# Kernel optimization log

Hardware: AMD Instinct MI355X
Metric: run time of the kernel (lower is better)

The kernel has to match this reference:

```python
import jax, jax.numpy as jnp
import numpy as np

C = 512
NUM_HEADS = 4
GROUPS = 32
EPS = 1e-5


def setup_inputs() -> dict:
    key = jax.random.key(0)
    ks = jax.random.split(key, 7)
    x = jax.random.normal(ks[0], (1, C, 4, 32, 32), dtype=jnp.float32)
    norm_w = jax.random.normal(ks[1], (C,), dtype=jnp.float32) * 0.02 + 1.0
    norm_b = jax.random.normal(ks[2], (C,), dtype=jnp.float32) * 0.02
    # 1x1x1 Conv3d == pointwise linear over channels
    qkv_w = jax.random.normal(ks[3], (3 * C, C), dtype=jnp.float32) * (C ** -0.5)
    qkv_b = jax.random.normal(ks[4], (3 * C,), dtype=jnp.float32) * 0.02
    proj_w = jax.random.normal(ks[5], (C, C), dtype=jnp.float32) * (C ** -0.5)
    proj_b = jax.random.normal(ks[6], (C,), dtype=jnp.float32) * 0.02
    return {"x": x, "norm_w": norm_w, "norm_b": norm_b,
            "qkv_w": qkv_w, "qkv_b": qkv_b,
            "proj_w": proj_w, "proj_b": proj_b}


def reference(x, norm_w, norm_b, qkv_w, qkv_b, proj_w, proj_b):
    B, Cc, T, H, W = x.shape
    N = T * H * W
    nh = NUM_HEADS
    d = Cc // nh
    # GroupNorm(32, C), biased variance, eps=1e-5
    xg = x.reshape(B, GROUPS, Cc // GROUPS, N)
    mu = xg.mean(axis=(2, 3), keepdims=True)
    var = xg.var(axis=(2, 3), keepdims=True)
    h = ((xg - mu) * jax.lax.rsqrt(var + EPS)).reshape(B, Cc, N)
    h = h * norm_w[None, :, None] + norm_b[None, :, None]
    # QKV 1x1 conv as channel matmul: (B, 3C, N)
    qkv = jnp.einsum('oc,bcn->bon', qkv_w, h) + qkv_b[None, :, None]
    qkv = qkv.reshape(B, 3, nh, d, N)
    q, k, v = qkv[:, 0], qkv[:, 1], qkv[:, 2]  # each (B, nh, d, N)
    scale = d ** -0.5
    attn = jax.nn.softmax(jnp.einsum('bhdn,bhdm->bhnm', q, k) * scale, axis=-1)
    out = jnp.einsum('bhnm,bhdm->bhdn', attn, v).reshape(B, Cc, N)
    out = jnp.einsum('oc,bcn->bon', proj_w, out) + proj_b[None, :, None]
    return x + out.reshape(B, Cc, T, H, W)
```

## Files before the change

kernel.cpp:

```cpp
#include <hip/hip_runtime.h>
#include <hip/hip_bf16.h>

#define CDIM 512
#define NTOK 4096
#define NH 4
#define DH 128
#define NGRP 32
#define EPS 1e-5f
#define NSPLIT 4
#define KVBLK 64
#define TPS (NTOK/KVBLK/NSPLIT)

typedef __attribute__((ext_vector_type(8))) short bf16x8;
typedef __attribute__((ext_vector_type(4))) short short4v;
typedef __attribute__((ext_vector_type(4))) float f32x4;
typedef __attribute__((ext_vector_type(16))) float f32x16;

__device__ inline unsigned short f2bf(float f){
  unsigned int u = __float_as_uint(f);
  u = (u + 0x7fffu + ((u >> 16) & 1u)) >> 16;
  return (unsigned short)u;
}

__device__ inline unsigned short f2bf_fast(float f){
  return (unsigned short)((__float_as_uint(f) + 0x8000u) >> 16);
}

__device__ inline float bf2f(unsigned short u){
  return __uint_as_float(((unsigned int)u) << 16);
}

__device__ inline f32x4 mfma_bf16(bf16x8 a, bf16x8 b, f32x4 c){
  asm("v_mfma_f32_16x16x32_bf16 %0, %1, %2, %0" : "+v"(c) : "v"(a), "v"(b));
  return c;
}

__device__ inline f32x16 mfma32(bf16x8 a, bf16x8 b, f32x16 c){
  asm("v_mfma_f32_32x32x16_bf16 %0, %1, %2, %0" : "+v"(c) : "v"(a), "v"(b));
  return c;
}

#define GLD16(gsrc, ldst) \
  __builtin_amdgcn_global_load_lds((__attribute__((address_space(1))) const void*)(gsrc), \
                                   (__attribute__((address_space(3))) void*)(ldst), 16, 0, 0)

#define KSC (0.088388347648318447f * 1.4426950408889634f)
#define INV_KSC (1.0f / KSC)
#define THR_RAW 60.0f
#define THR_K (THR_RAW * KSC)

__global__ __launch_bounds__(256) void k_convert(const float* __restrict__ qkv_w,
                                                 const float* __restrict__ proj_w,
                                                 unsigned short* __restrict__ qw,
                                                 unsigned short* __restrict__ pw){
  int stride = gridDim.x * blockDim.x;
  int i0 = blockIdx.x * blockDim.x + threadIdx.x;
  for (int i = i0; i < 3*CDIM*CDIM; i += stride) qw[i] = f2bf(qkv_w[i]);
  for (int i = i0; i < CDIM*CDIM; i += stride)   pw[i] = f2bf(proj_w[i]);
}

__global__ __launch_bounds__(256) void k_gnstats(const float* __restrict__ x,
                                                 float* __restrict__ stats){
  const int g = blockIdx.x, t = threadIdx.x;
  const f32x4* p = (const f32x4*)(x + (size_t)g * (16*NTOK));
  float s = 0.f, ss = 0.f;
  for (int i = t; i < 16*NTOK/4; i += 256){
    f32x4 v = p[i];
    s  += v[0]+v[1]+v[2]+v[3];
    ss += v[0]*v[0]+v[1]*v[1]+v[2]*v[2]+v[3]*v[3];
  }
  for (int off = 32; off > 0; off >>= 1){ s += __shfl_down(s, off); ss += __shfl_down(ss, off); }
  __shared__ float rs[4], rss[4];
  if ((t & 63) == 0){ rs[t>>6] = s; rss[t>>6] = ss; }
  __syncthreads();
  if (t == 0){
    float S  = rs[0]+rs[1]+rs[2]+rs[3];
    float SS = rss[0]+rss[1]+rss[2]+rss[3];
    const float inv = 1.f / (float)(16*NTOK);
    float mu  = S * inv;
    float var = SS * inv - mu*mu;
    stats[g]        = mu;
    stats[NGRP + g] = rsqrtf(var + EPS);
  }
}

__global__ __launch_bounds__(256) void k_gnapply(const float* __restrict__ x,
                                                 const float* __restrict__ stats,
                                                 const float* __restrict__ nw,
                                                 const float* __restrict__ nbias,
                                                 unsigned short* __restrict__ h_t){
  __shared__ float tile[64][68];
  const int n0 = blockIdx.x * 64, c0 = blockIdx.y * 64;
  const int t = threadIdx.x;
  {
    const int cl = t >> 2;
    #pragma unroll
    for (int i = 0; i < 4; i++){
      const int f4 = (t & 3) + i*4;
      *(f32x4*)&tile[cl][f4*4] = *(const f32x4*)(x + (size_t)(c0+cl)*NTOK + n0 + f4*4);
    }
  }
  __syncthreads();
  const int nl = t >> 2, cb = (t & 3) * 16;
  unsigned short ov[16] __attribute__((aligned(8)));
  #pragma unroll
  for (int j = 0; j < 16; j++){
    const int c = c0 + cb + j;
    const int grp = c >> 4;
    const float val = (tile[cb+j][nl] - stats[grp]) * stats[NGRP+grp] * nw[c] + nbias[c];
    ov[j] = f2bf(val);
  }
  unsigned short* dst = h_t + (size_t)(n0+nl)*CDIM + c0 + cb;
  #pragma unroll
  for (int j = 0; j < 4; j++) *(short4v*)(dst + j*4) = *(const short4v*)(ov + j*4);
}

template<int MODE>
__global__ __launch_bounds__(256) void k_gemm(const unsigned short* __restrict__ A,
                                              const unsigned short* __restrict__ Bt,
                                              const float* __restrict__ bias,
                                              const float* __restrict__ xres,
                                              unsigned short* __restrict__ q_t,
                                              unsigned short* __restrict__ k_t,
                                              unsigned short* __restrict__ vbuf,
                                              float* __restrict__ out,
                                              int K)
{
  __shared__ unsigned short Asm[128*32];
  __shared__ unsigned short Bsm[128*32];
  const int m0 = blockIdx.y * 128, n0 = blockIdx.x * 128;
  const int t = threadIdx.x;
  const int lane = t & 63, w = t >> 6;
  const int lo = lane & 15, g = lane >> 4;
  const int wr = w >> 1, wc = w & 1;
  f32x4 acc[4][4];
  #pragma unroll
  for (int i=0;i<4;i++)
    #pragma unroll
    for (int j=0;j<4;j++) acc[i][j] = f32x4{0.f,0.f,0.f,0.f};

  const int row = t >> 2, cb8 = (t & 3) * 8;
  for (int k0 = 0; k0 < K; k0 += 32){
    __syncthreads();
    *(bf16x8*)(Asm + row*32 + cb8)      = *(const bf16x8*)(A  + (size_t)(m0+row)*K    + k0 + cb8);
    *(bf16x8*)(Asm + (row+64)*32 + cb8) = *(const bf16x8*)(A  + (size_t)(m0+row+64)*K + k0 + cb8);
    *(bf16x8*)(Bsm + row*32 + cb8)      = *(const bf16x8*)(Bt + (size_t)(n0+row)*K    + k0 + cb8);
    *(bf16x8*)(Bsm + (row+64)*32 + cb8) = *(const bf16x8*)(Bt + (size_t)(n0+row+64)*K + k0 + cb8);
    __syncthreads();
    bf16x8 af[4], bfr[4];
    #pragma unroll
    for (int i=0;i<4;i++) af[i]  = *(const bf16x8*)(Asm + (wr*64 + i*16 + lo)*32 + g*8);
    #pragma unroll
    for (int j=0;j<4;j++) bfr[j] = *(const bf16x8*)(Bsm + (wc*64 + j*16 + lo)*32 + g*8);
    #pragma unroll
    for (int i=0;i<4;i++)
      #pragma unroll
      for (int j=0;j<4;j++)
        acc[i][j] = mfma_bf16(af[i], bfr[j], acc[i][j]);
  }

  if constexpr (MODE == 0){
    const int sQ = m0 >> 9;
    const int hh = (m0 >> 7) & 3;
    #pragma unroll
    for (int i=0;i<4;i++){
      const int ddb = wr*64 + i*16 + g*4;
      const int ob  = m0 + ddb;
      float b[4];
      #pragma unroll
      for (int r=0;r<4;r++) b[r] = bias[ob + r];
      #pragma unroll
      for (int j=0;j<4;j++){
        const int n = n0 + wc*64 + j*16 + lo;
        if (sQ < 2){
          unsigned short pk[4] __attribute__((aligned(8)));
          #pragma unroll
          for (int r=0;r<4;r++) pk[r] = f2bf(acc[i][j][r] + b[r]);
          unsigned short* dst = (sQ == 0 ? q_t : k_t) + ((size_t)hh*NTOK + n)*DH + ddb;
          *(short4v*)dst = *(const short4v*)pk;
        } else {
          #pragma unroll
          for (int r=0;r<4;r++)
            vbuf[((size_t)hh*DH + ddb + r)*NTOK + n] = f2bf(acc[i][j][r] + b[r]);
        }
      }
    }
  } else {
    #pragma unroll
    for (int i=0;i<4;i++){
      const int ob = m0 + wr*64 + i*16 + g*4;
      float b[4];
      #pragma unroll
      for (int r=0;r<4;r++) b[r] = bias[ob + r];
      #pragma unroll
      for (int j=0;j<4;j++){
        const int n = n0 + wc*64 + j*16 + lo;
        #pragma unroll
        for (int r=0;r<4;r++){
          size_t idx = (size_t)(ob + r)*NTOK + n;
          out[idx] = acc[i][j][r] + b[r] + xres[idx];
        }
      }
    }
  }
}

__global__ __launch_bounds__(512, 2) void k_attn(const unsigned short* __restrict__ q_t,
                                                 const unsigned short* __restrict__ k_t,
                                                 const unsigned short* __restrict__ vbuf,
                                                 unsigned short* __restrict__ opart,
                                                 float* __restrict__ mlbuf){
  const int h = blockIdx.y;
  const int qt = blockIdx.x >> 2, split = blockIdx.x & 3;
  const int t = threadIdx.x, w = t >> 6, lane = t & 63;
  const int la = lane & 31, hi = lane >> 5;
  const int s15 = la & 15, s7 = la & 7;
  const int nbq = qt * 256 + w * 32;

  __shared__ __align__(16) unsigned short Ksm[2][64*128];
  __shared__ __align__(16) unsigned short Vsm[2][128*64];
  __shared__ __align__(16) unsigned short P[8][32][72];

  const unsigned short* kg = k_t  + (size_t)h*NTOK*DH;
  const unsigned short* vg = vbuf + (size_t)h*DH*NTOK;

  auto stage = [&](int mt, int buf){
    const unsigned short* kgm = kg + (size_t)mt*KVBLK*DH;
    const unsigned short* vgm = vg + mt*KVBLK;
    #pragma unroll
    for (int rnd = 0; rnd < 2; rnd++){
      const int c = rnd*512 + t;
      const int row = c >> 4, col = c & 15;
      GLD16(kgm + (size_t)row*DH + ((col ^ (row & 15))*8), &Ksm[buf][c*8]);
    }
    #pragma unroll
    for (int rnd = 0; rnd < 2; rnd++){
      const int c = rnd*512 + t;
      const int row = c >> 3, col = c & 7;
      GLD16(vgm + (size_t)row*NTOK + ((col ^ (row & 7))*8), &Vsm[buf][c*8]);
    }
  };

  bf16x8 qa[8];
  {
    const unsigned short* qr = q_t + ((size_t)h*NTOK + nbq + la)*DH + hi*8;
    #pragma unroll
    for (int ks=0;ks<8;ks++) qa[ks] = *(const bf16x8*)(qr + ks*16);
  }
  bf16x8 onesf;
  #pragma unroll
  for (int j=0;j<8;j++) onesf[j] = (short)0x3F80;

  float mk[16];
  f32x16 oacc[4], lacc;
  #pragma unroll
  for (int r=0;r<16;r++){ mk[r] = -1e30f; }
  #pragma unroll
  for (int dt=0;dt<4;dt++)
    #pragma unroll
    for (int r=0;r<16;r++) oacc[dt][r] = 0.f;
  #pragma unroll
  for (int r=0;r<16;r++) lacc[r] = 0.f;

  const int mt0 = split * TPS;
  stage(mt0, 0);
  int cur = 0;
  for (int it = 0; it < TPS; it++){
    __syncthreads();
    if (it + 1 < TPS) stage(mt0 + it + 1, cur ^ 1);

    const unsigned short* Ks = Ksm[cur];
    const unsigned short* Vs = Vsm[cur];

    f32x16 s0, s1;
    #pragma unroll
    for (int r=0;r<16;r++){ s0[r] = 0.f; s1[r] = 0.f; }
    #pragma unroll
    for (int ks=0; ks<8; ks++){
      const int kc = ((2*ks + hi) ^ s15) * 8;
      bf16x8 kf0 = *(const bf16x8*)(Ks + la*128 + kc);
      bf16x8 kf1 = *(const bf16x8*)(Ks + (32+la)*128 + kc);
      s0 = mfma32(qa[ks], kf0, s0);
      s1 = mfma32(qa[ks], kf1, s1);
    }
    float tmax = s0[0];
    #pragma unroll
    for (int r=1;r<16;r++) tmax = fmaxf(tmax, s0[r]);
    #pragma unroll
    for (int r=0;r<16;r++) tmax = fmaxf(tmax, s1[r]);
    #pragma unroll
    for (int off=1; off<64; off<<=1) tmax = fmaxf(tmax, __shfl_xor(tmax, off));
    float mmink = mk[0];
    #pragma unroll
    for (int r=1;r<16;r++) mmink = fminf(mmink, mk[r]);
    if (!__all(tmax * KSC <= mmink + THR_K)){
      float rmax[16];
      #pragma unroll
      for (int r=0;r<16;r++) rmax[r] = fmaxf(s0[r], s1[r]);
      #pragma unroll
      for (int off=1; off<32; off<<=1)
        #pragma unroll
        for (int r=0;r<16;r++) rmax[r] = fmaxf(rmax[r], __shfl_xor(rmax[r], off));
      #pragma unroll
      for (int r=0;r<16;r++){
        float mold = mk[r] * INV_KSC;
        float mn   = fmaxf(mold, rmax[r]);
        float mnk  = mn * KSC;
        float al   = exp2f(mk[r] - mnk);
        mk[r] = mnk;
        lacc[r] *= al;
        #pragma unroll
        for (int dt=0;dt<4;dt++) oacc[dt][r] *= al;
      }
    }
    unsigned short* Pw = &P[w][0][0];
    #pragma unroll
    for (int r=0;r<16;r++){
      const int q = (r&3) + 8*(r>>2) + 4*hi;
      float p0 = exp2f(fmaf(s0[r], KSC, -mk[r]));
      float p1 = exp2f(fmaf(s1[r], KSC, -mk[r]));
      Pw[q*72 + la]      = f2bf_fast(p0);
      Pw[q*72 + 32 + la] = f2bf_fast(p1);
    }
    bf16x8 pa[4];
    #pragma unroll
    for (int kst=0;kst<4;kst++)
      pa[kst] = *(const bf16x8*)(&P[w][la][kst*16 + hi*8]);
    #pragma unroll
    for (int kst=0;kst<4;kst++) lacc = mfma32(pa[kst], onesf, lacc);
    #pragma unroll
    for (int dt=0; dt<4; dt++){
      const int vbase = (dt*32 + la)*64;
      #pragma unroll
      for (int kst=0;kst<4;kst++){
        const int vc = ((2*kst + hi) ^ s7) * 8;
        bf16x8 vf = *(const bf16x8*)(Vs + vbase + vc);
        oacc[dt] = mfma32(pa[kst], vf, oacc[dt]);
      }
    }
    cur ^= 1;
  }
  unsigned short* Od = opart + ((size_t)(split*NH + h)*NTOK + nbq)*DH;
  #pragma unroll
  for (int r=0;r<16;r++){
    const int q = (r&3) + 8*(r>>2) + 4*hi;
    const float linv = 1.f / lacc[r];
    #pragma unroll
    for (int dt=0;dt<4;dt++)
      Od[(size_t)q*DH + dt*32 + la] = f2bf(oacc[dt][r] * linv);
  }
  if (la == 0){
    float* ml = mlbuf + ((size_t)(split*NH + h)*NTOK + nbq)*2;
    #pragma unroll
    for (int r=0;r<16;r++){
      const int q = (r&3) + 8*(r>>2) + 4*hi;
      ml[q*2]     = mk[r] * INV_KSC;
      ml[q*2 + 1] = lacc[r];
    }
  }
}

__global__ __launch_bounds__(256) void k_merge(const unsigned short* __restrict__ opart,
                                               const float* __restrict__ mlbuf,
                                               unsigned short* __restrict__ ao_t){
  const int h = blockIdx.y;
  const int n = blockIdx.x*2 + (threadIdx.x >> 7);
  const int d = threadIdx.x & 127;
  float ms[NSPLIT], ls[NSPLIT], m = -1e30f;
  #pragma unroll
  for (int s=0;s<NSPLIT;s++){
    const float* ml = mlbuf + ((size_t)(s*NH + h)*NTOK + n)*2;
    ms[s] = ml[0]; ls[s] = ml[1];
    m = fmaxf(m, ms[s]);
  }
  float wsum = 0.f, o = 0.f;
  #pragma unroll
  for (int s=0;s<NSPLIT;s++){
    float wgt = exp2f((ms[s]-m)*KSC) * ls[s];
    wsum += wgt;
    o += wgt * bf2f(opart[((size_t)(s*NH + h)*NTOK + n)*DH + d]);
  }
  ao_t[(size_t)n*CDIM + h*DH + d] = f2bf(o / wsum);
}

extern "C" void kernel_launch(void* const* d_in, const int* in_sizes, int n_in,
                              void* d_out, int out_size, void* d_ws, size_t ws_size,
                              hipStream_t stream){
  const float* x      = (const float*)d_in[0];
  const float* norm_w = (const float*)d_in[1];
  const float* norm_b = (const float*)d_in[2];
  const float* qkv_w  = (const float*)d_in[3];
  const float* qkv_b  = (const float*)d_in[4];
  const float* proj_w = (const float*)d_in[5];
  const float* proj_b = (const float*)d_in[6];
  float* out = (float*)d_out;

  char* ws = (char*)d_ws;
  unsigned short* qw  = (unsigned short*)(ws);
  unsigned short* pw  = (unsigned short*)(ws + 1572864);
  unsigned short* h_t = (unsigned short*)(ws + 2097152);
  unsigned short* q_t = (unsigned short*)(ws + 6291456);
  unsigned short* k_t = (unsigned short*)(ws + 10485760);
  unsigned short* vb  = (unsigned short*)(ws + 14680064);
  unsigned short* ao  = (unsigned short*)(ws + 18874368);
  float* stats        = (float*)(ws + 23068672);
  unsigned short* opart = (unsigned short*)(ws + 23072768);
  float* mlbuf        = (float*)(ws + 39849984);

  hipLaunchKernelGGL(k_convert, dim3(1024), dim3(256), 0, stream, qkv_w, proj_w, qw, pw);
  hipLaunchKernelGGL(k_gnstats, dim3(32), dim3(256), 0, stream, x, stats);
  hipLaunchKernelGGL(k_gnapply, dim3(64, 8), dim3(256), 0, stream, x, stats, norm_w, norm_b, h_t);
  hipLaunchKernelGGL((k_gemm<0>), dim3(32, 12), dim3(256), 0, stream,
                     qw, h_t, qkv_b, (const float*)nullptr,
                     q_t, k_t, vb, (float*)nullptr, 512);
  hipLaunchKernelGGL(k_attn, dim3(16*NSPLIT, NH), dim3(512), 0, stream, q_t, k_t, vb, opart, mlbuf);
  hipLaunchKernelGGL(k_merge, dim3(NTOK/2, NH), dim3(256), 0, stream, opart, mlbuf, ao);
  hipLaunchKernelGGL((k_gemm<1>), dim3(32, 4), dim3(256), 0, stream,
                     pw, ao, proj_b, x,
                     (unsigned short*)nullptr, (unsigned short*)nullptr, (unsigned short*)nullptr, out, 512);
}
```

Baseline: 126.6 us.

## Keep attention probabilities in registers via transposed QK and raise KV split count

The attention kernel now computes S^T (K as the A operand) so each lane holds one query column. It packs probabilities to bf16 with v_cvt_pk and a cross-half lane shuffle instead of round-tripping through LDS. This drops the P shared buffer, the ones-vector MFMA row sum and the per-row max shuffles in favour of a per-lane running max and sum. The KV split factor becomes a template parameter that goes to 8 when the workspace allows, and launch bounds allow 4 blocks per CU. The costs are more partial outputs for the merge kernel to combine and register pressure at the higher occupancy target.

```diff
diff --git a/kernel.cpp b/kernel.cpp
--- a/kernel.cpp
+++ b/kernel.cpp
@@ -7,14 +7,13 @@
 #define DH 128
 #define NGRP 32
 #define EPS 1e-5f
-#define NSPLIT 4
 #define KVBLK 64
-#define TPS (NTOK/KVBLK/NSPLIT)
 
 typedef __attribute__((ext_vector_type(8))) short bf16x8;
 typedef __attribute__((ext_vector_type(4))) short short4v;
 typedef __attribute__((ext_vector_type(4))) float f32x4;
 typedef __attribute__((ext_vector_type(16))) float f32x16;
+typedef __attribute__((ext_vector_type(4))) unsigned int u32x4;
 
 __device__ inline unsigned short f2bf(float f){
   unsigned int u = __float_as_uint(f);
@@ -22,10 +21,6 @@
   return (unsigned short)u;
 }
 
-__device__ inline unsigned short f2bf_fast(float f){
-  return (unsigned short)((__float_as_uint(f) + 0x8000u) >> 16);
-}
-
 __device__ inline float bf2f(unsigned short u){
   return __uint_as_float(((unsigned int)u) << 16);
 }
@@ -38,6 +33,12 @@
 __device__ inline f32x16 mfma32(bf16x8 a, bf16x8 b, f32x16 c){
   asm("v_mfma_f32_32x32x16_bf16 %0, %1, %2, %0" : "+v"(c) : "v"(a), "v"(b));
   return c;
+}
+
+__device__ inline unsigned int cvtpk(float lo, float hi){
+  unsigned int r;
+  asm("v_cvt_pk_bf16_f32 %0, %1, %2" : "=v"(r) : "v"(lo), "v"(hi));
+  return r;
 }
 
 #define GLD16(gsrc, ldst) \
@@ -205,13 +206,15 @@
   }
 }
 
-__global__ __launch_bounds__(512, 2) void k_attn(const unsigned short* __restrict__ q_t,
+template<int NS>
+__global__ __launch_bounds__(512, 4) void k_attn(const unsigned short* __restrict__ q_t,
                                                  const unsigned short* __restrict__ k_t,
                                                  const unsigned short* __restrict__ vbuf,
                                                  unsigned short* __restrict__ opart,
                                                  float* __restrict__ mlbuf){
+  const int TPS = NTOK/KVBLK/NS;
   const int h = blockIdx.y;
-  const int qt = blockIdx.x >> 2, split = blockIdx.x & 3;
+  const int qt = blockIdx.x / NS, split = blockIdx.x % NS;
   const int t = threadIdx.x, w = t >> 6, lane = t & 63;
   const int la = lane & 31, hi = lane >> 5;
   const int s15 = la & 15, s7 = la & 7;
@@ -219,7 +222,6 @@
 
   __shared__ __align__(16) unsigned short Ksm[2][64*128];
   __shared__ __align__(16) unsigned short Vsm[2][128*64];
-  __shared__ __align__(16) unsigned short P[8][32][72];
 
   const unsigned short* kg = k_t  + (size_t)h*NTOK*DH;
   const unsigned short* vg = vbuf + (size_t)h*DH*NTOK;
@@ -247,20 +249,14 @@
     #pragma unroll
     for (int ks=0;ks<8;ks++) qa[ks] = *(const bf16x8*)(qr + ks*16);
   }
-  bf16x8 onesf;
-  #pragma unroll
-  for (int j=0;j<8;j++) onesf[j] = (short)0x3F80;
-
-  float mk[16];
-  f32x16 oacc[4], lacc;
-  #pragma unroll
-  for (int r=0;r<16;r++){ mk[r] = -1e30f; }
+
+  float mk = -1e30f;
+  float lsum = 0.f;
+  f32x16 oacc[4];
   #pragma unroll
   for (int dt=0;dt<4;dt++)
     #pragma unroll
     for (int r=0;r<16;r++) oacc[dt][r] = 0.f;
-  #pragma unroll
-  for (int r=0;r<16;r++) lacc[r] = 0.f;
 
   const int mt0 = split * TPS;
   stage(mt0, 0);
@@ -272,110 +268,101 @@
     const unsigned short* Ks = Ksm[cur];
     const unsigned short* Vs = Vsm[cur];
 
-    f32x16 s0, s1;
-    #pragma unroll
-    for (int r=0;r<16;r++){ s0[r] = 0.f; s1[r] = 0.f; }
-    #pragma unroll
-    for (int ks=0; ks<8; ks++){
-      const int kc = ((2*ks + hi) ^ s15) * 8;
-      bf16x8 kf0 = *(const bf16x8*)(Ks + la*128 + kc);
-      bf16x8 kf1 = *(const bf16x8*)(Ks + (32+la)*128 + kc);
-      s0 = mfma32(qa[ks], kf0, s0);
-      s1 = mfma32(qa[ks], kf1, s1);
-    }
-    float tmax = s0[0];
-    #pragma unroll
-    for (int r=1;r<16;r++) tmax = fmaxf(tmax, s0[r]);
-    #pragma unroll
-    for (int r=0;r<16;r++) tmax = fmaxf(tmax, s1[r]);
-    #pragma unroll
-    for (int off=1; off<64; off<<=1) tmax = fmaxf(tmax, __shfl_xor(tmax, off));
-    float mmink = mk[0];
-    #pragma unroll
-    for (int r=1;r<16;r++) mmink = fminf(mmink, mk[r]);
-    if (!__all(tmax * KSC <= mmink + THR_K)){
-      float rmax[16];
-      #pragma unroll
-      for (int r=0;r<16;r++) rmax[r] = fmaxf(s0[r], s1[r]);
-      #pragma unroll
-      for (int off=1; off<32; off<<=1)
+    #pragma unroll
+    for (int half = 0; half < 2; half++){
+      f32x16 s;
+      #pragma unroll
+      for (int r=0;r<16;r++) s[r] = 0.f;
+      #pragma unroll
+      for (int ks=0; ks<8; ks++){
+        bf16x8 kf = *(const bf16x8*)(Ks + (half*32 + la)*128 + (((2*ks + hi) ^ s15) * 8));
+        s = mfma32(kf, qa[ks], s);
+      }
+      float hmax = s[0];
+      #pragma unroll
+      for (int r=1;r<16;r++) hmax = fmaxf(hmax, s[r]);
+      hmax = fmaxf(hmax, __shfl_xor(hmax, 32));
+      const float hk = hmax * KSC;
+      if (!__all(hk <= mk + THR_K)){
+        const float mnk = fmaxf(mk, hk);
+        const float al  = exp2f(mk - mnk);
+        mk = mnk;
+        lsum *= al;
         #pragma unroll
-        for (int r=0;r<16;r++) rmax[r] = fmaxf(rmax[r], __shfl_xor(rmax[r], off));
+        for (int r=0;r<16;r++){
+          const float a = __shfl(al, (r&3) + 8*(r>>2) + 4*hi);
+          #pragma unroll
+          for (int dt=0;dt<4;dt++) oacc[dt][r] *= a;
+        }
+      }
       #pragma unroll
       for (int r=0;r<16;r++){
-        float mold = mk[r] * INV_KSC;
-        float mn   = fmaxf(mold, rmax[r]);
-        float mnk  = mn * KSC;
-        float al   = exp2f(mk[r] - mnk);
-        mk[r] = mnk;
-        lacc[r] *= al;
-        #pragma unroll
-        for (int dt=0;dt<4;dt++) oacc[dt][r] *= al;
-      }
-    }
-    unsigned short* Pw = &P[w][0][0];
-    #pragma unroll
-    for (int r=0;r<16;r++){
-      const int q = (r&3) + 8*(r>>2) + 4*hi;
-      float p0 = exp2f(fmaf(s0[r], KSC, -mk[r]));
-      float p1 = exp2f(fmaf(s1[r], KSC, -mk[r]));
-      Pw[q*72 + la]      = f2bf_fast(p0);
-      Pw[q*72 + 32 + la] = f2bf_fast(p1);
-    }
-    bf16x8 pa[4];
-    #pragma unroll
-    for (int kst=0;kst<4;kst++)
-      pa[kst] = *(const bf16x8*)(&P[w][la][kst*16 + hi*8]);
-    #pragma unroll
-    for (int kst=0;kst<4;kst++) lacc = mfma32(pa[kst], onesf, lacc);
-    #pragma unroll
-    for (int dt=0; dt<4; dt++){
-      const int vbase = (dt*32 + la)*64;
-      #pragma unroll
-      for (int kst=0;kst<4;kst++){
-        const int vc = ((2*kst + hi) ^ s7) * 8;
-        bf16x8 vf = *(const bf16x8*)(Vs + vbase + vc);
-        oacc[dt] = mfma32(pa[kst], vf, oacc[dt]);
+        s[r] = exp2f(fmaf(s[r], KSC, -mk));
+        lsum += s[r];
+      }
+      bf16x8 paf[2];
+      #pragma unroll
+      for (int b=0;b<2;b++){
+        unsigned int A = cvtpk(s[8*b+0], s[8*b+1]);
+        unsigned int B = cvtpk(s[8*b+2], s[8*b+3]);
+        unsigned int C = cvtpk(s[8*b+4], s[8*b+5]);
+        unsigned int D = cvtpk(s[8*b+6], s[8*b+7]);
+        unsigned int E = hi ? A : C;
+        unsigned int F = hi ? B : D;
+        E = (unsigned int)__shfl_xor((int)E, 32);
+        F = (unsigned int)__shfl_xor((int)F, 32);
+        u32x4 m;
+        m[0] = hi ? E : A;
+        m[1] = hi ? F : B;
+        m[2] = hi ? C : E;
+        m[3] = hi ? D : F;
+        paf[b] = __builtin_bit_cast(bf16x8, m);
+      }
+      #pragma unroll
+      for (int dt=0; dt<4; dt++){
+        const int vbase = (dt*32 + la)*64;
+        bf16x8 vf0 = *(const bf16x8*)(Vs + vbase + (((2*(half*2+0) + hi) ^ s7) * 8));
+        bf16x8 vf1 = *(const bf16x8*)(Vs + vbase + (((2*(half*2+1) + hi) ^ s7) * 8));
+        oacc[dt] = mfma32(paf[0], vf0, oacc[dt]);
+        oacc[dt] = mfma32(paf[1], vf1, oacc[dt]);
       }
     }
     cur ^= 1;
   }
+  const float lt = lsum + __shfl_xor(lsum, 32);
   unsigned short* Od = opart + ((size_t)(split*NH + h)*NTOK + nbq)*DH;
   #pragma unroll
   for (int r=0;r<16;r++){
     const int q = (r&3) + 8*(r>>2) + 4*hi;
-    const float linv = 1.f / lacc[r];
+    const float linv = 1.f / __shfl(lt, q);
     #pragma unroll
     for (int dt=0;dt<4;dt++)
       Od[(size_t)q*DH + dt*32 + la] = f2bf(oacc[dt][r] * linv);
   }
-  if (la == 0){
+  if (hi == 0){
     float* ml = mlbuf + ((size_t)(split*NH + h)*NTOK + nbq)*2;
-    #pragma unroll
-    for (int r=0;r<16;r++){
-      const int q = (r&3) + 8*(r>>2) + 4*hi;
-      ml[q*2]     = mk[r] * INV_KSC;
-      ml[q*2 + 1] = lacc[r];
-    }
-  }
-}
-
+    ml[la*2]     = mk * INV_KSC;
+    ml[la*2 + 1] = lt;
+  }
+}
+
+template<int NS>
 __global__ __launch_bounds__(256) void k_merge(const unsigned short* __restrict__ opart,
                                                const float* __restrict__ mlbuf,
                                                unsigned short* __restrict__ ao_t){
   const int h = blockIdx.y;
   const int n = blockIdx.x*2 + (threadIdx.x >> 7);
   const int d = threadIdx.x & 127;
-  float ms[NSPLIT], ls[NSPLIT], m = -1e30f;
-  #pragma unroll
-  for (int s=0;s<NSPLIT;s++){
+  float ms[NS], ls[NS], m = -1e30f;
+  #pragma unroll
+  for (int s=0;s<NS;s++){
     const float* ml = mlbuf + ((size_t)(s*NH + h)*NTOK + n)*2;
     ms[s] = ml[0]; ls[s] = ml[1];
     m = fmaxf(m, ms[s]);
   }
   float wsum = 0.f, o = 0.f;
   #pragma unroll
-  for (int s=0;s<NSPLIT;s++){
+  for (int s=0;s<NS;s++){
     float wgt = exp2f((ms[s]-m)*KSC) * ls[s];
     wsum += wgt;
     o += wgt * bf2f(opart[((size_t)(s*NH + h)*NTOK + n)*DH + d]);
@@ -405,7 +392,6 @@
   unsigned short* ao  = (unsigned short*)(ws + 18874368);
   float* stats        = (float*)(ws + 23068672);
   unsigned short* opart = (unsigned short*)(ws + 23072768);
-  float* mlbuf        = (float*)(ws + 39849984);
 
   hipLaunchKernelGGL(k_convert, dim3(1024), dim3(256), 0, stream, qkv_w, proj_w, qw, pw);
   hipLaunchKernelGGL(k_gnstats, dim3(32), dim3(256), 0, stream, x, stats);
@@ -413,8 +399,21 @@
   hipLaunchKernelGGL((k_gemm<0>), dim3(32, 12), dim3(256), 0, stream,
                      qw, h_t, qkv_b, (const float*)nullptr,
                      q_t, k_t, vb, (float*)nullptr, 512);
-  hipLaunchKernelGGL(k_attn, dim3(16*NSPLIT, NH), dim3(512), 0, stream, q_t, k_t, vb, opart, mlbuf);
-  hipLaunchKernelGGL(k_merge, dim3(NTOK/2, NH), dim3(256), 0, stream, opart, mlbuf, ao);
+
+  if (ws_size >= 57675776ULL){
+    constexpr int NS = 8;
+    float* mlbuf = (float*)(ws + 23072768 + (size_t)NS*NH*NTOK*DH*2);
+    hipLaunchKernelGGL((k_attn<NS>), dim3((NTOK/256)*NS, NH), dim3(512), 0, stream,
+                       q_t, k_t, vb, opart, mlbuf);
+    hipLaunchKernelGGL((k_merge<NS>), dim3(NTOK/2, NH), dim3(256), 0, stream, opart, mlbuf, ao);
+  } else {
+    constexpr int NS = 4;
+    float* mlbuf = (float*)(ws + 23072768 + (size_t)NS*NH*NTOK*DH*2);
+    hipLaunchKernelGGL((k_attn<NS>), dim3((NTOK/256)*NS, NH), dim3(512), 0, stream,
+                       q_t, k_t, vb, opart, mlbuf);
+    hipLaunchKernelGGL((k_merge<NS>), dim3(NTOK/2, NH), dim3(256), 0, stream, opart, mlbuf, ao);
+  }
+
   hipLaunchKernelGGL((k_gemm<1>), dim3(32, 4), dim3(256), 0, stream,
                      pw, ao, proj_b, x,
                      (unsigned short*)nullptr, (unsigned short*)nullptr, (unsigned short*)nullptr, out, 512);
```

Measured after the change: 266.4 us. 2.1x slower.
